# Kernel tuning notes

Hardware: AMD Instinct MI355X
Metric: run time of the kernel (lower is better)

## Reference

```python
import jax, jax.numpy as jnp
import numpy as np

B = 4096
D = 256
N = 9000000
ALPHA = 0.5      # alpha_weight
GAMMA_S = 0.8
GAMMA_U = 0.9
RHO = 6.0
EPS = 1e-14
ETA = 0.01
TAU_MIN = 0.001
TAU_MAX = 1.0
GRAD_CLIP = 5.0
TAU_INIT = 0.07


def setup_inputs() -> dict:
    key = jax.random.key(0)
    k1, k2 = jax.random.split(key)
    return {
        "zis": jax.random.normal(k1, (B, D), dtype=jnp.float32),
        "zjs": jax.random.normal(k2, (B, D), dtype=jnp.float32),
        "ids": jnp.arange(B, dtype=jnp.int32),
        "s_I": jnp.zeros(N, jnp.float32),
        "s_T": jnp.zeros(N, jnp.float32),
        "b_I": jnp.zeros(N, jnp.float32),
        "b_T": jnp.zeros(N, jnp.float32),
        "u_I": jnp.zeros(N, jnp.float32),
        "u_T": jnp.zeros(N, jnp.float32),
        "tau_I": jnp.full(N, TAU_INIT, jnp.float32),
        "tau_T": jnp.full(N, TAU_INIT, jnp.float32),
    }


def reference(zis, zjs, ids, s_I, s_T, b_I, b_T, u_I, u_T, tau_I, tau_T):
    sg = jax.lax.stop_gradient
    Bc = zis.shape[0]
    # normalize
    zis = zis / jnp.linalg.norm(zis, axis=1, keepdims=True)
    zjs = zjs / jnp.linalg.norm(zjs, axis=1, keepdims=True)
    sim = jnp.einsum('id,jd->ij', zis, zjs)                 # [B,B]
    diag = jnp.diagonal(sim)
    image_diffs = sim - diag[:, None]
    text_diffs = sim - diag[None, :]
    tau_i = tau_I[ids]
    tau_t = tau_T[ids]
    # detached temperature-scaled diffs (torch .detach())
    idt = sg(image_diffs) / tau_i[:, None]
    tdt = sg(text_diffs) / tau_t[None, :]
    # running max update (online log-sum-exp shift)
    old_b_i = b_I[ids]
    old_b_t = b_T[ids]
    new_b_i = jnp.maximum(old_b_i, idt.max(axis=1))
    new_b_t = jnp.maximum(old_b_t, tdt.max(axis=0))
    mask = 1.0 - jnp.eye(Bc, dtype=zis.dtype)
    exp_i = jnp.exp(idt - new_b_i[:, None]) * mask
    exp_t = jnp.exp(tdt - new_b_t[None, :]) * mask
    g_i = exp_i.sum(axis=1)                                  # [B]
    g_t = exp_t.sum(axis=0)                                  # [B]
    # EMA of normalizers, rescaled by max shift
    s_i = (1.0 - GAMMA_S) * s_I[ids] * jnp.exp(old_b_i - new_b_i) + GAMMA_S * g_i
    s_t = (1.0 - GAMMA_S) * s_T[ids] * jnp.exp(old_b_t - new_b_t) + GAMMA_S * g_t
    s_i_c = jnp.clip(s_i, EPS, None)[:, None]                # [B,1]
    s_t_c = jnp.clip(s_t, EPS, None)[None, :]                # [1,B]
    w_i = exp_i / s_i_c
    w_t = exp_t / s_t_c
    image_loss = (sg(w_i) * image_diffs).sum(axis=1)         # [B]
    text_loss = (sg(w_t) * text_diffs).sum(axis=0)           # [B]
    total_loss = ALPHA * image_loss.mean() + (1.0 - ALPHA) * text_loss.mean()
    grad_tau_image = jnp.log(s_i_c) + new_b_i[:, None] + RHO - (w_i * idt).sum(axis=1, keepdims=True) / (Bc - 1)
    grad_tau_text = jnp.log(s_t_c) + new_b_t[None, :] + RHO - (w_t * tdt).sum(axis=0, keepdims=True) / (Bc - 1)
    # EMA of tau gradients with clipping, then temperature update
    u_i = (1.0 - GAMMA_U) * u_I[ids] + GAMMA_U * jnp.clip(grad_tau_image[:, 0], -GRAD_CLIP, GRAD_CLIP)
    u_t = (1.0 - GAMMA_U) * u_T[ids] + GAMMA_U * jnp.clip(grad_tau_text[0, :], -GRAD_CLIP, GRAD_CLIP)
    tau_i_new = jnp.clip(tau_i - ETA * u_i, TAU_MIN, TAU_MAX)
    tau_t_new = jnp.clip(tau_t - ETA * u_t, TAU_MIN, TAU_MAX)
    # scatter updated state back into persistent buffers
    s_I = s_I.at[ids].set(s_i)
    s_T = s_T.at[ids].set(s_t)
    b_I = b_I.at[ids].set(new_b_i)
    b_T = b_T.at[ids].set(new_b_t)
    u_I = u_I.at[ids].set(u_i)
    u_T = u_T.at[ids].set(u_t)
    tau_I = tau_I.at[ids].set(tau_i_new)
    tau_T = tau_T.at[ids].set(tau_t_new)
    return (g_i[:, None], g_t[None, :], grad_tau_image, grad_tau_text, total_loss,
            tau_i.mean(), tau_t.mean(), s_I, s_T, b_I, b_T, u_I, u_T, tau_I, tau_T)
```

## Files before the change

kernel.cpp:

```cpp
#include <hip/hip_runtime.h>
#include <math.h>

#define BDIM 4096
#define DDIM 256
#define NSTATE 9000000

#define C_ALPHA 0.5f
#define C_GAMMA_S 0.8f
#define C_GAMMA_U 0.9f
#define C_RHO 6.0f
#define C_EPS 1e-14f
#define C_ETA 0.01f
#define C_TAU_MIN 0.001f
#define C_TAU_MAX 1.0f
#define C_GRAD_CLIP 5.0f

__global__ __launch_bounds__(256) void kinv(const float* __restrict__ zis,
                                            const float* __restrict__ zjs,
                                            float* __restrict__ invnI,
                                            float* __restrict__ invnJ) {
    int row = blockIdx.x;
    int t = threadIdx.x;
    const float* src = (row < BDIM) ? zis + (size_t)row * DDIM
                                    : zjs + (size_t)(row - BDIM) * DDIM;
    float v = src[t];
    __shared__ float red[256];
    red[t] = v * v;
    __syncthreads();
    for (int s = 128; s > 0; s >>= 1) {
        if (t < s) red[t] += red[t + s];
        __syncthreads();
    }
    if (t == 0) {
        float inv = rsqrtf(red[0]);
        if (row < BDIM) invnI[row] = inv; else invnJ[row - BDIM] = inv;
    }
}

__global__ __launch_bounds__(256) void ktau(const int* __restrict__ ids,
                                            const float* __restrict__ tau_I,
                                            const float* __restrict__ tau_T,
                                            float* __restrict__ rowIT,
                                            float* __restrict__ colIT) {
    int i = blockIdx.x * 256 + threadIdx.x;
    if (i >= BDIM) return;
    int id = ids[i];
    rowIT[i] = 1.0f / tau_I[id];
    colIT[i] = 1.0f / tau_T[id];
}

#define BMT 128
#define BNT 128
#define BKT 16

__device__ inline int rowIdxOf(int ty, int mi) { return ty * 4 + (mi & 3) + ((mi >> 2) << 6); }
__device__ inline int colIdxOf(int tx, int ni) { return tx * 4 + (ni & 3) + ((ni >> 2) << 6); }

__global__ __launch_bounds__(256) void kgemm(
    const float* __restrict__ ZA, const float* __restrict__ ZB,
    const float* __restrict__ invA, const float* __restrict__ invB,
    const float* __restrict__ rowIT, const float* __restrict__ colIT,
    float* __restrict__ rPM, float* __restrict__ rPS1, float* __restrict__ rPS2,
    float* __restrict__ cPM, float* __restrict__ cPS1, float* __restrict__ cPS2,
    float* __restrict__ diag)
{
    __shared__ float As[BKT][BMT + 4];
    __shared__ float Bs[BKT][BNT + 4];

    int bx = blockIdx.x, by = blockIdx.y;
    int t = threadIdx.x;
    int tx = t & 15, ty = t >> 4;
    int m0 = by * BMT, n0 = bx * BNT;
    int kq = (t & 3) * 4;
    int lrow = t >> 2;
    int w = t >> 6;

    float ivA0 = invA[m0 + lrow], ivA1 = invA[m0 + lrow + 64];
    float ivB0 = invB[n0 + lrow], ivB1 = invB[n0 + lrow + 64];

    float acc[8][8];
#pragma unroll
    for (int a = 0; a < 8; a++)
#pragma unroll
        for (int b = 0; b < 8; b++) acc[a][b] = 0.f;

    for (int k0 = 0; k0 < DDIM; k0 += BKT) {
        float4 a0 = *(const float4*)&ZA[(size_t)(m0 + lrow) * DDIM + k0 + kq];
        float4 a1 = *(const float4*)&ZA[(size_t)(m0 + lrow + 64) * DDIM + k0 + kq];
        float4 b0 = *(const float4*)&ZB[(size_t)(n0 + lrow) * DDIM + k0 + kq];
        float4 b1 = *(const float4*)&ZB[(size_t)(n0 + lrow + 64) * DDIM + k0 + kq];
        a0.x *= ivA0; a0.y *= ivA0; a0.z *= ivA0; a0.w *= ivA0;
        a1.x *= ivA1; a1.y *= ivA1; a1.z *= ivA1; a1.w *= ivA1;
        b0.x *= ivB0; b0.y *= ivB0; b0.z *= ivB0; b0.w *= ivB0;
        b1.x *= ivB1; b1.y *= ivB1; b1.z *= ivB1; b1.w *= ivB1;
        __syncthreads();
        As[kq + 0][lrow] = a0.x; As[kq + 1][lrow] = a0.y; As[kq + 2][lrow] = a0.z; As[kq + 3][lrow] = a0.w;
        As[kq + 0][lrow + 64] = a1.x; As[kq + 1][lrow + 64] = a1.y; As[kq + 2][lrow + 64] = a1.z; As[kq + 3][lrow + 64] = a1.w;
        Bs[kq + 0][lrow] = b0.x; Bs[kq + 1][lrow] = b0.y; Bs[kq + 2][lrow] = b0.z; Bs[kq + 3][lrow] = b0.w;
        Bs[kq + 0][lrow + 64] = b1.x; Bs[kq + 1][lrow + 64] = b1.y; Bs[kq + 2][lrow + 64] = b1.z; Bs[kq + 3][lrow + 64] = b1.w;
        __syncthreads();
#pragma unroll
        for (int k = 0; k < BKT; k++) {
            float4 t0 = *(const float4*)&As[k][ty * 4];
            float4 t1 = *(const float4*)&As[k][ty * 4 + 64];
            float4 t2 = *(const float4*)&Bs[k][tx * 4];
            float4 t3 = *(const float4*)&Bs[k][tx * 4 + 64];
            float am[8] = {t0.x, t0.y, t0.z, t0.w, t1.x, t1.y, t1.z, t1.w};
            float bn[8] = {t2.x, t2.y, t2.z, t2.w, t3.x, t3.y, t3.z, t3.w};
#pragma unroll
            for (int mi = 0; mi < 8; mi++)
#pragma unroll
                for (int ni = 0; ni < 8; ni++)
                    acc[mi][ni] = fmaf(am[mi], bn[ni], acc[mi][ni]);
        }
    }

#pragma unroll
    for (int mi = 0; mi < 8; mi++) {
        int r = m0 + rowIdxOf(ty, mi);
        float it = rowIT[r];
        float m = acc[mi][0];
#pragma unroll
        for (int ni = 1; ni < 8; ni++) m = fmaxf(m, acc[mi][ni]);
#pragma unroll
        for (int off = 1; off < 16; off <<= 1) m = fmaxf(m, __shfl_xor(m, off));
        float s1 = 0.f, s2 = 0.f;
#pragma unroll
        for (int ni = 0; ni < 8; ni++) {
            float v = acc[mi][ni];
            float e = __expf((v - m) * it);
            s1 += e; s2 += e * v;
        }
#pragma unroll
        for (int off = 1; off < 16; off <<= 1) { s1 += __shfl_xor(s1, off); s2 += __shfl_xor(s2, off); }
        if (tx == 0) {
            rPM [bx * BDIM + r] = m;
            rPS1[bx * BDIM + r] = s1;
            rPS2[bx * BDIM + r] = s2;
        }
    }

#pragma unroll
    for (int ni = 0; ni < 8; ni++) {
        int c = n0 + colIdxOf(tx, ni);
        float it = colIT[c];
        float m = acc[0][ni];
#pragma unroll
        for (int mi = 1; mi < 8; mi++) m = fmaxf(m, acc[mi][ni]);
        float s1 = 0.f, s2 = 0.f;
#pragma unroll
        for (int mi = 0; mi < 8; mi++) {
            float v = acc[mi][ni];
            float e = __expf((v - m) * it);
            s1 += e; s2 += e * v;
        }
#pragma unroll
        for (int off = 16; off < 64; off <<= 1) {
            float mo  = __shfl_xor(m, off);
            float s1o = __shfl_xor(s1, off);
            float s2o = __shfl_xor(s2, off);
            float M = fmaxf(m, mo);
            float ea = __expf((m - M) * it);
            float eb = __expf((mo - M) * it);
            s1 = s1 * ea + s1o * eb;
            s2 = s2 * ea + s2o * eb;
            m = M;
        }
        if ((t & 48) == 0) {
            int slot = by * 4 + w;
            cPM [slot * BDIM + c] = m;
            cPS1[slot * BDIM + c] = s1;
            cPS2[slot * BDIM + c] = s2;
        }
    }

    if (bx == by && tx == ty) {
#pragma unroll
        for (int mi = 0; mi < 8; mi++) diag[m0 + rowIdxOf(ty, mi)] = acc[mi][mi];
    }
}

__global__ __launch_bounds__(256) void kmerge(
    const int* __restrict__ ids,
    const float* __restrict__ s_I, const float* __restrict__ b_I,
    const float* __restrict__ u_I, const float* __restrict__ tau_I,
    const float* __restrict__ s_T, const float* __restrict__ b_T,
    const float* __restrict__ u_T, const float* __restrict__ tau_T,
    const float* __restrict__ rowIT, const float* __restrict__ colIT,
    const float* __restrict__ diag,
    const float* __restrict__ rPM, const float* __restrict__ rPS1, const float* __restrict__ rPS2,
    const float* __restrict__ cPM, const float* __restrict__ cPS1, const float* __restrict__ cPS2,
    float* __restrict__ O,
    float* __restrict__ sc_arrs,
    float* __restrict__ img_loss_arr,
    float* __restrict__ txt_loss_arr)
{
    int j = blockIdx.x * 256 + threadIdx.x;
    if (j >= 2 * BDIM) return;
    bool rowside = (j < BDIM);
    int i = rowside ? j : j - BDIM;
    const float* PM  = rowside ? rPM  : cPM;
    const float* PS1 = rowside ? rPS1 : cPS1;
    const float* PS2 = rowside ? rPS2 : cPS2;
    int K = rowside ? 32 : 128;
    float it = rowside ? rowIT[i] : colIT[i];

    float M = -INFINITY, S1 = 0.f, S2 = 0.f;
    for (int k = 0; k < K; k++) {
        float m  = PM [k * BDIM + i];
        float s1 = PS1[k * BDIM + i];
        float s2 = PS2[k * BDIM + i];
        float Mn = fmaxf(M, m);
        float ea = __expf((M - Mn) * it);
        float eb = __expf((m - Mn) * it);
        S1 = S1 * ea + s1 * eb;
        S2 = S2 * ea + s2 * eb;
        M = Mn;
    }

    int id = ids[i];
    float tau  = rowside ? tau_I[id] : tau_T[id];
    float oldb = rowside ? b_I[id]   : b_T[id];
    float olds = rowside ? s_I[id]   : s_T[id];
    float oldu = rowside ? u_I[id]   : u_T[id];
    float dg = diag[i];

    float nb = fmaxf(oldb, (M - dg) * it);
    float F  = __expf((M - dg) * it - nb);
    float ed = __expf(-nb);
    float g  = F * S1 - ed;
    float Cs = F * (S2 - dg * S1);

    float s_new = (1.f - C_GAMMA_S) * olds * __expf(oldb - nb) + C_GAMMA_S * g;
    float sc = fmaxf(s_new, C_EPS);
    float loss = Cs / sc;
    float grad = logf(sc) + nb + C_RHO - (Cs / (sc * tau)) * (1.0f / (float)(BDIM - 1));
    float gc = fminf(fmaxf(grad, -C_GRAD_CLIP), C_GRAD_CLIP);
    float u_new = (1.f - C_GAMMA_U) * oldu + C_GAMMA_U * gc;
    float tau_new = fminf(fmaxf(tau - C_ETA * u_new, C_TAU_MIN), C_TAU_MAX);

    if (rowside) {
        O[i] = g;
        O[8192 + i] = grad;
        sc_arrs[0 * BDIM + i] = s_new;
        sc_arrs[1 * BDIM + i] = nb;
        sc_arrs[2 * BDIM + i] = u_new;
        sc_arrs[3 * BDIM + i] = tau_new;
        img_loss_arr[i] = loss;
    } else {
        O[4096 + i] = g;
        O[12288 + i] = grad;
        sc_arrs[4 * BDIM + i] = s_new;
        sc_arrs[5 * BDIM + i] = nb;
        sc_arrs[6 * BDIM + i] = u_new;
        sc_arrs[7 * BDIM + i] = tau_new;
        txt_loss_arr[i] = loss;
    }
}

__global__ __launch_bounds__(256) void kscalars(const float* __restrict__ img_loss_arr,
                                                const float* __restrict__ txt_loss_arr,
                                                const int* __restrict__ ids,
                                                const float* __restrict__ tau_I,
                                                const float* __restrict__ tau_T,
                                                float* __restrict__ O) {
    int t = threadIdx.x;
    float s0 = 0.f, s1 = 0.f, s2 = 0.f, s3 = 0.f;
    for (int k = t; k < BDIM; k += 256) {
        s0 += img_loss_arr[k];
        s1 += txt_loss_arr[k];
        int id = ids[k];
        s2 += tau_I[id];
        s3 += tau_T[id];
    }
    __shared__ float r0[256], r1[256], r2[256], r3[256];
    r0[t] = s0; r1[t] = s1; r2[t] = s2; r3[t] = s3;
    __syncthreads();
    for (int s = 128; s > 0; s >>= 1) {
        if (t < s) {
            r0[t] += r0[t + s]; r1[t] += r1[t + s];
            r2[t] += r2[t + s]; r3[t] += r3[t + s];
        }
        __syncthreads();
    }
    if (t == 0) {
        float invB = 1.0f / (float)BDIM;
        O[16384] = C_ALPHA * (r0[0] * invB) + (1.f - C_ALPHA) * (r1[0] * invB);
        O[16385] = r2[0] * invB;
        O[16386] = r3[0] * invB;
    }
}

__global__ __launch_bounds__(256) void kcopy(const float* __restrict__ s_I,
                                             const float* __restrict__ s_T,
                                             const float* __restrict__ b_I,
                                             const float* __restrict__ b_T,
                                             const float* __restrict__ u_I,
                                             const float* __restrict__ u_T,
                                             const float* __restrict__ tau_I,
                                             const float* __restrict__ tau_T,
                                             float* __restrict__ o) {
    const float4* srcs[8] = {(const float4*)s_I, (const float4*)s_T,
                             (const float4*)b_I, (const float4*)b_T,
                             (const float4*)u_I, (const float4*)u_T,
                             (const float4*)tau_I, (const float4*)tau_T};
    long tid = (long)blockIdx.x * 256 + threadIdx.x;
#pragma unroll
    for (int b = 0; b < 8; b++) {
        const float4* s = srcs[b];
        float* d = o + (long)b * NSTATE;
        for (long k = tid; k < NSTATE / 4; k += 2097152) {
            float4 v = s[k];
            float* dp = d + 4 * k;
            dp[0] = v.x; dp[1] = v.y; dp[2] = v.z; dp[3] = v.w;
        }
    }
}

__global__ __launch_bounds__(256) void kscatter(const int* __restrict__ ids,
                                                const float* __restrict__ sc_arrs,
                                                float* __restrict__ o) {
    int t = blockIdx.x * 256 + threadIdx.x;
    if (t >= BDIM) return;
    long id = ids[t];
    o[0L * NSTATE + id] = sc_arrs[0 * BDIM + t];
    o[1L * NSTATE + id] = sc_arrs[4 * BDIM + t];
    o[2L * NSTATE + id] = sc_arrs[1 * BDIM + t];
    o[3L * NSTATE + id] = sc_arrs[5 * BDIM + t];
    o[4L * NSTATE + id] = sc_arrs[2 * BDIM + t];
    o[5L * NSTATE + id] = sc_arrs[6 * BDIM + t];
    o[6L * NSTATE + id] = sc_arrs[3 * BDIM + t];
    o[7L * NSTATE + id] = sc_arrs[7 * BDIM + t];
}

extern "C" void kernel_launch(void* const* d_in, const int* in_sizes, int n_in,
                              void* d_out, int out_size, void* d_ws, size_t ws_size,
                              hipStream_t stream) {
    const float* zis   = (const float*)d_in[0];
    const float* zjs   = (const float*)d_in[1];
    const int*   ids   = (const int*)d_in[2];
    const float* s_I   = (const float*)d_in[3];
    const float* s_T   = (const float*)d_in[4];
    const float* b_I   = (const float*)d_in[5];
    const float* b_T   = (const float*)d_in[6];
    const float* u_I   = (const float*)d_in[7];
    const float* u_T   = (const float*)d_in[8];
    const float* tau_I = (const float*)d_in[9];
    const float* tau_T = (const float*)d_in[10];
    float* O  = (float*)d_out;
    float* ws = (float*)d_ws;

    float* pBase = O + 16388;
    float* rPM  = pBase;
    float* rPS1 = pBase + 131072;
    float* rPS2 = pBase + 262144;
    float* cPM  = pBase + 393216;
    float* cPS1 = pBase + 917504;
    float* cPS2 = pBase + 1441792;

    float* invnI  = ws;
    float* invnJ  = ws + 4096;
    float* rowIT  = ws + 8192;
    float* colIT  = ws + 12288;
    float* diag   = ws + 16384;
    float* sc_arrs = ws + 20480;
    float* img_loss_arr = ws + 53248;
    float* txt_loss_arr = ws + 57344;

    kinv<<<2 * BDIM, 256, 0, stream>>>(zis, zjs, invnI, invnJ);
    ktau<<<16, 256, 0, stream>>>(ids, tau_I, tau_T, rowIT, colIT);

    kgemm<<<dim3(32, 32), 256, 0, stream>>>(zis, zjs, invnI, invnJ, rowIT, colIT,
                                            rPM, rPS1, rPS2, cPM, cPS1, cPS2, diag);

    kmerge<<<32, 256, 0, stream>>>(ids, s_I, b_I, u_I, tau_I, s_T, b_T, u_T, tau_T,
                                   rowIT, colIT, diag,
                                   rPM, rPS1, rPS2, cPM, cPS1, cPS2,
                                   O, sc_arrs, img_loss_arr, txt_loss_arr);

    kscalars<<<1, 256, 0, stream>>>(img_loss_arr, txt_loss_arr, ids, tau_I, tau_T, O);

    kcopy<<<8192, 256, 0, stream>>>(s_I, s_T, b_I, b_T, u_I, u_T, tau_I, tau_T, O + 16387);

    kscatter<<<16, 256, 0, stream>>>(ids, sc_arrs, O + 16387);
}
```

Measured before the change: 678.8 us.

## Replace FP32 SIMT GEMM with split-bf16 MFMA and fused normalization prep

Adds a prep kernel that normalizes rows and splits each value into high and low bf16 parts, stored in an MFMA-friendly packed layout. This replaces the separate norm kernel. The similarity GEMM now uses 32x32x16 bf16 MFMA with three products (hh, hl, lh) to stay close to fp32 accuracy, instead of scalar FMA. The epilogue is reorganized: column partials are reduced within the wave, and row partials go through an LDS transpose. Partial-slot counts change to 64 on both sides. The risk is a small precision loss from the bf16x3 emulation, and the 9M-element state copy still dominates total time.

New measurement: 557.0 us. 1.22x faster.

```diff
diff --git a/kernel.cpp b/kernel.cpp
--- a/kernel.cpp
+++ b/kernel.cpp
@@ -15,27 +15,18 @@
 #define C_TAU_MAX 1.0f
 #define C_GRAD_CLIP 5.0f
 
-__global__ __launch_bounds__(256) void kinv(const float* __restrict__ zis,
-                                            const float* __restrict__ zjs,
-                                            float* __restrict__ invnI,
-                                            float* __restrict__ invnJ) {
-    int row = blockIdx.x;
-    int t = threadIdx.x;
-    const float* src = (row < BDIM) ? zis + (size_t)row * DDIM
-                                    : zjs + (size_t)(row - BDIM) * DDIM;
-    float v = src[t];
-    __shared__ float red[256];
-    red[t] = v * v;
-    __syncthreads();
-    for (int s = 128; s > 0; s >>= 1) {
-        if (t < s) red[t] += red[t + s];
-        __syncthreads();
-    }
-    if (t == 0) {
-        float inv = rsqrtf(red[0]);
-        if (row < BDIM) invnI[row] = inv; else invnJ[row - BDIM] = inv;
-    }
-}
+typedef unsigned short u16;
+typedef __attribute__((ext_vector_type(8))) short short8;
+typedef __attribute__((ext_vector_type(16))) float f32x16;
+
+#define MFMA32 __builtin_amdgcn_mfma_f32_32x32x16_bf16
+
+__device__ inline u16 f2bf(float f) {
+    unsigned u = __float_as_uint(f);
+    unsigned r = (u + 0x7FFFu + ((u >> 16) & 1u)) >> 16;
+    return (u16)r;
+}
+__device__ inline float bf2f(u16 h) { return __uint_as_float(((unsigned)h) << 16); }
 
 __global__ __launch_bounds__(256) void ktau(const int* __restrict__ ids,
                                             const float* __restrict__ tau_I,
@@ -49,135 +40,173 @@
     colIT[i] = 1.0f / tau_T[id];
 }
 
-#define BMT 128
-#define BNT 128
-#define BKT 16
-
-__device__ inline int rowIdxOf(int ty, int mi) { return ty * 4 + (mi & 3) + ((mi >> 2) << 6); }
-__device__ inline int colIdxOf(int tx, int ni) { return tx * 4 + (ni & 3) + ((ni >> 2) << 6); }
-
-__global__ __launch_bounds__(256) void kgemm(
-    const float* __restrict__ ZA, const float* __restrict__ ZB,
-    const float* __restrict__ invA, const float* __restrict__ invB,
+__global__ __launch_bounds__(256) void kprep(const float* __restrict__ zis,
+                                             const float* __restrict__ zjs,
+                                             u16* __restrict__ Ah, u16* __restrict__ Al,
+                                             u16* __restrict__ Bh, u16* __restrict__ Bl) {
+    int blk = blockIdx.x;
+    bool isB = blk >= 128;
+    const float* Z = isB ? zjs : zis;
+    u16* H = isB ? Bh : Ah;
+    u16* L = isB ? Bl : Al;
+    int rblk = blk & 127;
+    int t = threadIdx.x;
+    int r = t & 31, kc0 = t >> 5;
+    int row = rblk * 32 + r;
+
+    __shared__ float ssq[32];
+    if (t < 32) ssq[t] = 0.f;
+    __syncthreads();
+
+    float4 v[8];
+    float partial = 0.f;
+#pragma unroll
+    for (int c = 0; c < 4; ++c) {
+        int kc = kc0 + 8 * c;
+        float4 a = *(const float4*)&Z[(size_t)row * DDIM + kc * 8];
+        float4 b = *(const float4*)&Z[(size_t)row * DDIM + kc * 8 + 4];
+        v[2 * c] = a; v[2 * c + 1] = b;
+        partial += a.x * a.x + a.y * a.y + a.z * a.z + a.w * a.w;
+        partial += b.x * b.x + b.y * b.y + b.z * b.z + b.w * b.w;
+    }
+    atomicAdd(&ssq[r], partial);
+    __syncthreads();
+    float inv = rsqrtf(ssq[r]);
+
+#pragma unroll
+    for (int c = 0; c < 4; ++c) {
+        int kc = kc0 + 8 * c;
+        float f[8];
+        f[0] = v[2*c].x * inv;   f[1] = v[2*c].y * inv;
+        f[2] = v[2*c].z * inv;   f[3] = v[2*c].w * inv;
+        f[4] = v[2*c+1].x * inv; f[5] = v[2*c+1].y * inv;
+        f[6] = v[2*c+1].z * inv; f[7] = v[2*c+1].w * inv;
+        u16 hh[8], ll[8];
+#pragma unroll
+        for (int j = 0; j < 8; ++j) {
+            hh[j] = f2bf(f[j]);
+            ll[j] = f2bf(f[j] - bf2f(hh[j]));
+        }
+        size_t base = (size_t)rblk * 8192 + (size_t)kc * 256 + (size_t)r * 8;
+        uint4 ph, pl;
+        ph.x = (unsigned)hh[0] | ((unsigned)hh[1] << 16);
+        ph.y = (unsigned)hh[2] | ((unsigned)hh[3] << 16);
+        ph.z = (unsigned)hh[4] | ((unsigned)hh[5] << 16);
+        ph.w = (unsigned)hh[6] | ((unsigned)hh[7] << 16);
+        pl.x = (unsigned)ll[0] | ((unsigned)ll[1] << 16);
+        pl.y = (unsigned)ll[2] | ((unsigned)ll[3] << 16);
+        pl.z = (unsigned)ll[4] | ((unsigned)ll[5] << 16);
+        pl.w = (unsigned)ll[6] | ((unsigned)ll[7] << 16);
+        *(uint4*)(H + base) = ph;
+        *(uint4*)(L + base) = pl;
+    }
+}
+
+__global__ __launch_bounds__(256, 3) void kgemm(
+    const u16* __restrict__ Ah, const u16* __restrict__ Al,
+    const u16* __restrict__ Bh, const u16* __restrict__ Bl,
     const float* __restrict__ rowIT, const float* __restrict__ colIT,
     float* __restrict__ rPM, float* __restrict__ rPS1, float* __restrict__ rPS2,
     float* __restrict__ cPM, float* __restrict__ cPS1, float* __restrict__ cPS2,
     float* __restrict__ diag)
 {
-    __shared__ float As[BKT][BMT + 4];
-    __shared__ float Bs[BKT][BNT + 4];
+    __shared__ float T[2][64 * 68];
 
     int bx = blockIdx.x, by = blockIdx.y;
     int t = threadIdx.x;
-    int tx = t & 15, ty = t >> 4;
-    int m0 = by * BMT, n0 = bx * BNT;
-    int kq = (t & 3) * 4;
-    int lrow = t >> 2;
-    int w = t >> 6;
-
-    float ivA0 = invA[m0 + lrow], ivA1 = invA[m0 + lrow + 64];
-    float ivB0 = invB[n0 + lrow], ivB1 = invB[n0 + lrow + 64];
-
-    float acc[8][8];
+    int w = t >> 6, l = t & 63;
+    int rw = w & 1, cw = w >> 1;
+    int h = l >> 5, lc = l & 31;
+    int rowbase = by * 128 + rw * 64;
+    int colbase = bx * 128 + cw * 64;
+
+    const u16* pAh = Ah + (size_t)(by * 4 + rw * 2) * 8192;
+    const u16* pAl = Al + (size_t)(by * 4 + rw * 2) * 8192;
+    const u16* pBh = Bh + (size_t)(bx * 4 + cw * 2) * 8192;
+    const u16* pBl = Bl + (size_t)(bx * 4 + cw * 2) * 8192;
+
+    f32x16 acc00, acc01, acc10, acc11;
 #pragma unroll
-    for (int a = 0; a < 8; a++)
-#pragma unroll
-        for (int b = 0; b < 8; b++) acc[a][b] = 0.f;
-
-    for (int k0 = 0; k0 < DDIM; k0 += BKT) {
-        float4 a0 = *(const float4*)&ZA[(size_t)(m0 + lrow) * DDIM + k0 + kq];
-        float4 a1 = *(const float4*)&ZA[(size_t)(m0 + lrow + 64) * DDIM + k0 + kq];
-        float4 b0 = *(const float4*)&ZB[(size_t)(n0 + lrow) * DDIM + k0 + kq];
-        float4 b1 = *(const float4*)&ZB[(size_t)(n0 + lrow + 64) * DDIM + k0 + kq];
-        a0.x *= ivA0; a0.y *= ivA0; a0.z *= ivA0; a0.w *= ivA0;
-        a1.x *= ivA1; a1.y *= ivA1; a1.z *= ivA1; a1.w *= ivA1;
-        b0.x *= ivB0; b0.y *= ivB0; b0.z *= ivB0; b0.w *= ivB0;
-        b1.x *= ivB1; b1.y *= ivB1; b1.z *= ivB1; b1.w *= ivB1;
-        __syncthreads();
-        As[kq + 0][lrow] = a0.x; As[kq + 1][lrow] = a0.y; As[kq + 2][lrow] = a0.z; As[kq + 3][lrow] = a0.w;
-        As[kq + 0][lrow + 64] = a1.x; As[kq + 1][lrow + 64] = a1.y; As[kq + 2][lrow + 64] = a1.z; As[kq + 3][lrow + 64] = a1.w;
-        Bs[kq + 0][lrow] = b0.x; Bs[kq + 1][lrow] = b0.y; Bs[kq + 2][lrow] = b0.z; Bs[kq + 3][lrow] = b0.w;
-        Bs[kq + 0][lrow + 64] = b1.x; Bs[kq + 1][lrow + 64] = b1.y; Bs[kq + 2][lrow + 64] = b1.z; Bs[kq + 3][lrow + 64] = b1.w;
-        __syncthreads();
-#pragma unroll
-        for (int k = 0; k < BKT; k++) {
-            float4 t0 = *(const float4*)&As[k][ty * 4];
-            float4 t1 = *(const float4*)&As[k][ty * 4 + 64];
-            float4 t2 = *(const float4*)&Bs[k][tx * 4];
-            float4 t3 = *(const float4*)&Bs[k][tx * 4 + 64];
-            float am[8] = {t0.x, t0.y, t0.z, t0.w, t1.x, t1.y, t1.z, t1.w};
-            float bn[8] = {t2.x, t2.y, t2.z, t2.w, t3.x, t3.y, t3.z, t3.w};
-#pragma unroll
-            for (int mi = 0; mi < 8; mi++)
-#pragma unroll
-                for (int ni = 0; ni < 8; ni++)
-                    acc[mi][ni] = fmaf(am[mi], bn[ni], acc[mi][ni]);
-        }
-    }
-
-#pragma unroll
-    for (int mi = 0; mi < 8; mi++) {
-        int r = m0 + rowIdxOf(ty, mi);
-        float it = rowIT[r];
-        float m = acc[mi][0];
-#pragma unroll
-        for (int ni = 1; ni < 8; ni++) m = fmaxf(m, acc[mi][ni]);
-#pragma unroll
-        for (int off = 1; off < 16; off <<= 1) m = fmaxf(m, __shfl_xor(m, off));
-        float s1 = 0.f, s2 = 0.f;
-#pragma unroll
-        for (int ni = 0; ni < 8; ni++) {
-            float v = acc[mi][ni];
-            float e = __expf((v - m) * it);
-            s1 += e; s2 += e * v;
-        }
-#pragma unroll
-        for (int off = 1; off < 16; off <<= 1) { s1 += __shfl_xor(s1, off); s2 += __shfl_xor(s2, off); }
-        if (tx == 0) {
-            rPM [bx * BDIM + r] = m;
-            rPS1[bx * BDIM + r] = s1;
-            rPS2[bx * BDIM + r] = s2;
-        }
-    }
-
-#pragma unroll
-    for (int ni = 0; ni < 8; ni++) {
-        int c = n0 + colIdxOf(tx, ni);
-        float it = colIT[c];
-        float m = acc[0][ni];
-#pragma unroll
-        for (int mi = 1; mi < 8; mi++) m = fmaxf(m, acc[mi][ni]);
-        float s1 = 0.f, s2 = 0.f;
-#pragma unroll
-        for (int mi = 0; mi < 8; mi++) {
-            float v = acc[mi][ni];
-            float e = __expf((v - m) * it);
-            s1 += e; s2 += e * v;
-        }
-#pragma unroll
-        for (int off = 16; off < 64; off <<= 1) {
-            float mo  = __shfl_xor(m, off);
-            float s1o = __shfl_xor(s1, off);
-            float s2o = __shfl_xor(s2, off);
-            float M = fmaxf(m, mo);
-            float ea = __expf((m - M) * it);
-            float eb = __expf((mo - M) * it);
-            s1 = s1 * ea + s1o * eb;
-            s2 = s2 * ea + s2o * eb;
-            m = M;
-        }
-        if ((t & 48) == 0) {
-            int slot = by * 4 + w;
-            cPM [slot * BDIM + c] = m;
-            cPS1[slot * BDIM + c] = s1;
-            cPS2[slot * BDIM + c] = s2;
-        }
-    }
-
-    if (bx == by && tx == ty) {
-#pragma unroll
-        for (int mi = 0; mi < 8; mi++) diag[m0 + rowIdxOf(ty, mi)] = acc[mi][mi];
-    }
+    for (int e = 0; e < 16; ++e) { acc00[e] = 0.f; acc01[e] = 0.f; acc10[e] = 0.f; acc11[e] = 0.f; }
+
+    for (int s = 0; s < 16; ++s) {
+        int off = s * 512 + l * 8;
+        short8 a0h = *(const short8*)(pAh + off);
+        short8 a1h = *(const short8*)(pAh + 8192 + off);
+        short8 a0l = *(const short8*)(pAl + off);
+        short8 a1l = *(const short8*)(pAl + 8192 + off);
+        short8 b0h = *(const short8*)(pBh + off);
+        short8 b1h = *(const short8*)(pBh + 8192 + off);
+        short8 b0l = *(const short8*)(pBl + off);
+        short8 b1l = *(const short8*)(pBl + 8192 + off);
+
+        acc00 = MFMA32(a0h, b0h, acc00, 0, 0, 0);
+        acc01 = MFMA32(a0h, b1h, acc01, 0, 0, 0);
+        acc10 = MFMA32(a1h, b0h, acc10, 0, 0, 0);
+        acc11 = MFMA32(a1h, b1h, acc11, 0, 0, 0);
+        acc00 = MFMA32(a0h, b0l, acc00, 0, 0, 0);
+        acc01 = MFMA32(a0h, b1l, acc01, 0, 0, 0);
+        acc10 = MFMA32(a1h, b0l, acc10, 0, 0, 0);
+        acc11 = MFMA32(a1h, b1l, acc11, 0, 0, 0);
+        acc00 = MFMA32(a0l, b0h, acc00, 0, 0, 0);
+        acc01 = MFMA32(a0l, b1h, acc01, 0, 0, 0);
+        acc10 = MFMA32(a1l, b0h, acc10, 0, 0, 0);
+        acc11 = MFMA32(a1l, b1h, acc11, 0, 0, 0);
+    }
+
+#define COLPART(A0, A1, CT) do {                                                   \
+        int gc = colbase + (CT) * 32 + lc;                                         \
+        float itc = colIT[gc];                                                     \
+        float m = -INFINITY;                                                       \
+        _Pragma("unroll") for (int e = 0; e < 16; ++e) {                           \
+            m = fmaxf(m, (A0)[e]); m = fmaxf(m, (A1)[e]); }                        \
+        m = fmaxf(m, __shfl_xor(m, 32));                                           \
+        float S1 = 0.f, S2 = 0.f;                                                  \
+        _Pragma("unroll") for (int e = 0; e < 16; ++e) {                           \
+            float v0 = (A0)[e]; float e0 = __expf((v0 - m) * itc); S1 += e0; S2 += e0 * v0; \
+            float v1 = (A1)[e]; float e1 = __expf((v1 - m) * itc); S1 += e1; S2 += e1 * v1; } \
+        S1 += __shfl_xor(S1, 32); S2 += __shfl_xor(S2, 32);                        \
+        if (h == 0) { int slot = by * 2 + rw;                                      \
+            cPM [slot * 4096 + gc] = m;                                            \
+            cPS1[slot * 4096 + gc] = S1;                                           \
+            cPS2[slot * 4096 + gc] = S2; }                                         \
+    } while (0)
+
+    COLPART(acc00, acc10, 0);
+    COLPART(acc01, acc11, 1);
+
+#define ROWPART(TB) do {                                                           \
+        float* Tb = (TB);                                                          \
+        _Pragma("unroll") for (int q = 0; q < 4; ++q) {                            \
+            _Pragma("unroll") for (int j = 0; j < 4; ++j) {                        \
+                int rr = 8 * q + 4 * h + j;                                        \
+                Tb[(rr     ) * 68 + lc     ] = acc00[4 * q + j];                   \
+                Tb[(rr     ) * 68 + lc + 32] = acc01[4 * q + j];                   \
+                Tb[(rr + 32) * 68 + lc     ] = acc10[4 * q + j];                   \
+                Tb[(rr + 32) * 68 + lc + 32] = acc11[4 * q + j]; } }               \
+        float itr = rowIT[rowbase + l];                                            \
+        float4 vv[16];                                                             \
+        _Pragma("unroll") for (int c = 0; c < 16; ++c)                             \
+            vv[c] = *(const float4*)&Tb[l * 68 + 4 * c];                           \
+        float m = -INFINITY;                                                       \
+        _Pragma("unroll") for (int c = 0; c < 16; ++c)                             \
+            m = fmaxf(m, fmaxf(fmaxf(vv[c].x, vv[c].y), fmaxf(vv[c].z, vv[c].w))); \
+        float S1 = 0.f, S2 = 0.f;                                                  \
+        _Pragma("unroll") for (int c = 0; c < 16; ++c) {                           \
+            float e0 = __expf((vv[c].x - m) * itr); S1 += e0; S2 += e0 * vv[c].x;  \
+            float e1 = __expf((vv[c].y - m) * itr); S1 += e1; S2 += e1 * vv[c].y;  \
+            float e2 = __expf((vv[c].z - m) * itr); S1 += e2; S2 += e2 * vv[c].z;  \
+            float e3 = __expf((vv[c].w - m) * itr); S1 += e3; S2 += e3 * vv[c].w; }\
+        int slot = bx * 2 + cw;                                                    \
+        rPM [slot * 4096 + rowbase + l] = m;                                       \
+        rPS1[slot * 4096 + rowbase + l] = S1;                                      \
+        rPS2[slot * 4096 + rowbase + l] = S2;                                      \
+        if (bx == by && rw == cw) diag[rowbase + l] = Tb[l * 68 + l];              \
+    } while (0)
+
+    if (w < 2) ROWPART(T[w]);
+    __syncthreads();
+    if (w >= 2) ROWPART(T[w - 2]);
 }
 
 __global__ __launch_bounds__(256) void kmerge(
@@ -202,11 +231,10 @@
     const float* PM  = rowside ? rPM  : cPM;
     const float* PS1 = rowside ? rPS1 : cPS1;
     const float* PS2 = rowside ? rPS2 : cPS2;
-    int K = rowside ? 32 : 128;
     float it = rowside ? rowIT[i] : colIT[i];
 
     float M = -INFINITY, S1 = 0.f, S2 = 0.f;
-    for (int k = 0; k < K; k++) {
+    for (int k = 0; k < 64; k++) {
         float m  = PM [k * BDIM + i];
         float s1 = PS1[k * BDIM + i];
         float s2 = PS2[k * BDIM + i];
@@ -350,27 +378,30 @@
     float* O  = (float*)d_out;
     float* ws = (float*)d_ws;
 
-    float* pBase = O + 16388;
-    float* rPM  = pBase;
-    float* rPS1 = pBase + 131072;
-    float* rPS2 = pBase + 262144;
-    float* cPM  = pBase + 393216;
-    float* cPS1 = pBase + 917504;
-    float* cPS2 = pBase + 1441792;
-
-    float* invnI  = ws;
-    float* invnJ  = ws + 4096;
-    float* rowIT  = ws + 8192;
-    float* colIT  = ws + 12288;
-    float* diag   = ws + 16384;
-    float* sc_arrs = ws + 20480;
-    float* img_loss_arr = ws + 53248;
-    float* txt_loss_arr = ws + 57344;
-
-    kinv<<<2 * BDIM, 256, 0, stream>>>(zis, zjs, invnI, invnJ);
+    float* P = O + 16388;
+    float* rPM  = P;
+    float* rPS1 = P + 262144;
+    float* rPS2 = P + 524288;
+    float* cPM  = P + 786432;
+    float* cPS1 = P + 1048576;
+    float* cPS2 = P + 1310720;
+    float* diag = P + 1572864;
+    u16* AB = (u16*)(P + 1576960);
+    u16* Ah = AB;
+    u16* Al = AB + 1048576;
+    u16* Bh = AB + 2097152;
+    u16* Bl = AB + 3145728;
+
+    float* rowIT  = ws;
+    float* colIT  = ws + 4096;
+    float* sc_arrs = ws + 8192;
+    float* img_loss_arr = ws + 40960;
+    float* txt_loss_arr = ws + 45056;
+
     ktau<<<16, 256, 0, stream>>>(ids, tau_I, tau_T, rowIT, colIT);
-
-    kgemm<<<dim3(32, 32), 256, 0, stream>>>(zis, zjs, invnI, invnJ, rowIT, colIT,
+    kprep<<<256, 256, 0, stream>>>(zis, zjs, Ah, Al, Bh, Bl);
+
+    kgemm<<<dim3(32, 32), 256, 0, stream>>>(Ah, Al, Bh, Bl, rowIT, colIT,
                                             rPM, rPS1, rPS2, cPM, cPS1, cPS2, diag);
 
     kmerge<<<32, 256, 0, stream>>>(ids, s_I, b_I, u_I, tau_I, s_T, b_T, u_T, tau_T,
```
